# Performance work log

Hardware: AMD Instinct MI355X
Metric: run time of the kernel (lower is better)

The kernel has to match this reference:

```python
import jax, jax.numpy as jnp
import numpy as np

L, N, D, T = 24, 576, 4096, 128
RED = D // 4           # DSU reduced dim (reduction_ratio=4)
FOCUS = (-2) % L       # focus layer index = 22
EPS_LN = 1e-5          # torch LayerNorm default eps
EPS_SC = 1e-6          # score-normalization eps
N_FOCUS = 32           # final_focus (hardcoded in forward)
N_NONFOCUS = 32        # final_nonfocus (hardcoded in forward)
MIN_ACTIVE = 8
THRESH = 3.0


def _ln(x, g=None, b=None):
    mu = x.mean(-1, keepdims=True)
    var = ((x - mu) ** 2).mean(-1, keepdims=True)
    y = (x - mu) / jnp.sqrt(var + EPS_LN)
    if g is not None:
        y = y * g + b
    return y


def setup_inputs() -> dict:
    key = jax.random.key(0)
    ks = jax.random.split(key, 10)
    rn = lambda k, shape, s=0.02: jax.random.normal(k, shape, jnp.float32) * s
    z = lambda n: jnp.zeros((n,), jnp.float32)
    return {
        'text_features': jax.random.normal(ks[0], (T, D), jnp.float32),
        'layer_feats': jax.random.normal(ks[1], (L, N, D), jnp.float32),
        'W1': rn(ks[2], (RED, 3 * D)), 'b1': z(RED),
        'Wc': rn(ks[3], (D, RED)), 'bc_lin': z(D), 'bc': z(D),
        'Wi': rn(ks[4], (D, RED)), 'bi_lin': z(D), 'bi': z(D),
        'Wf': rn(ks[5], (D, RED)), 'bf_lin': z(D), 'bf': z(D),
        'score_q_w': rn(ks[6], (D, D)), 'score_k_w': rn(ks[7], (D, D)),
        'ln_g': jnp.ones((D,), jnp.float32), 'ln_b': z(D),
        'layer_logits': rn(ks[8], (L,), 0.1),
        'scale': jnp.array([0.1], jnp.float32),
    }


def reference(text_features, layer_feats, W1, b1, Wc, bc_lin, bc, Wi, bi_lin, bi,
              Wf, bf_lin, bf, score_q_w, score_k_w, ln_g, ln_b, layer_logits, scale):
    # --- text conditioning ---
    text_global = _ln(text_features.mean(0))                 # [D]
    y = layer_feats.mean(1)                                   # [L, D] per-layer pooled

    # --- DSU recurrence over layers (LSTM-like cell) ---
    def dsu(c_prev, y_l):
        comb = jnp.concatenate([jax.nn.sigmoid(c_prev), y_l, text_global])
        s = jax.nn.relu(W1 @ comb + b1)                       # [RED]
        c_t = jnp.tanh(Wc @ s + bc_lin + bc)
        i = jax.nn.sigmoid(Wi @ s + bi_lin + bi)
        f = jax.nn.sigmoid(Wf @ s + bf_lin + bf)
        c = f * c_prev + i * c_t
        return c, c

    _, ctx = jax.lax.scan(dsu, jnp.zeros((D,), text_features.dtype), y)  # [L, D]

    # --- per-layer scores with LayerNorm'd q/k ---
    q = _ln(ctx @ score_q_w.T, ln_g, ln_b)                    # [L, D]
    kf = _ln(layer_feats @ score_k_w.T, ln_g, ln_b)           # [L, N, D]
    raw = jnp.einsum('lnd,ld->ln', kf, q)                     # [L, N]
    mu = raw.mean(1, keepdims=True)
    sd = raw.std(1, keepdims=True) + EPS_SC                   # unbiased=False
    scores = (raw - mu) / sd                                  # [L, N]
    conf = scores.max(1)                                      # [L]

    # --- active-layer selection (threshold path vs top-8 fallback) ---
    nonfocus = jnp.ones((L,), bool).at[FOCUS].set(False)
    conf_nf = jnp.where(nonfocus, conf, -jnp.inf)
    act_t = nonfocus & (conf > THRESH)
    M_t = act_t.sum()
    _, idx_f = jax.lax.top_k(conf_nf, MIN_ACTIVE)             # fallback: top-8 conf, desc
    act_f = jnp.zeros((L,), bool).at[idx_f].set(True)
    pos_f = jnp.full((L,), L, jnp.int32).at[idx_f].set(jnp.arange(MIN_ACTIVE, dtype=jnp.int32))
    pos_t = jnp.cumsum(act_t.astype(jnp.int32)) - 1           # ascending layer order
    use_fb = M_t < MIN_ACTIVE
    act = jnp.where(use_fb, act_f, act_t)
    pos = jnp.where(use_fb, pos_f, pos_t)
    M = jnp.where(use_fb, MIN_ACTIVE, M_t)

    # --- budget split: base per active layer + remainder to earliest (N=576 >> 32, no deficit) ---
    base = N_NONFOCUS // M
    rem = N_NONFOCUS - base * M
    k_nf = jnp.where(act, base + (pos < rem).astype(jnp.int32), 0)  # [L], sums to 32

    # --- per-layer top-32 indices (sorted desc), gather evidence ---
    _, top_idx = jax.lax.top_k(scores, N_FOCUS)               # [L, 32]
    ev_focus = layer_feats[FOCUS][top_idx[FOCUS]]             # [32, D]
    cum = jnp.cumsum(k_nf)                                    # [L]
    t = jnp.arange(N_NONFOCUS)
    li = jnp.searchsorted(cum, t, side='right')               # owning layer per slot
    r = t - (cum[li] - k_nf[li])                              # rank within layer
    ev_nf = layer_feats[li, top_idx[li, r]]                   # [32, D]

    # --- anchor-residual layer mix + 3x3 group pooling ---
    logits = layer_logits.astype(jnp.float32).at[FOCUS].set(-jnp.inf)
    alpha = jax.nn.softmax(logits)                            # [L], alpha[anchor]=0
    anchor = layer_feats[FOCUS]                               # [N, D]
    delta = jnp.einsum('l,lnd->nd', alpha, layer_feats - anchor[None])
    x_mix = anchor + scale[0] * delta                         # [576, D]
    groups = x_mix.reshape(3, 8, 3, 8, D).transpose(0, 2, 1, 3, 4).reshape(9, 64, D).mean(1)

    return jnp.concatenate([ev_focus, ev_nf, groups], 0)      # [73, D]
```

## Files before the change

kernel.cpp:

```cpp
#include <hip/hip_runtime.h>
#include <stdint.h>
#include <math.h>

#define LAY 24
#define NTOK 576
#define DIM 4096
#define TTXT 128
#define REDD 1024
#define FOCUSL 22

typedef unsigned int u32;
typedef unsigned short u16;
typedef float f32x4 __attribute__((ext_vector_type(4)));
typedef short bf16x8 __attribute__((ext_vector_type(8)));
typedef u16 u16x4 __attribute__((ext_vector_type(4)));

__device__ __forceinline__ u16 f2bf(float f) {
  u32 u = __builtin_bit_cast(u32, f);
  u32 r = u + 0x7fffu + ((u >> 16) & 1u);
  return (u16)(r >> 16);
}
__device__ __forceinline__ float sigm(float x) { return 1.0f / (1.0f + expf(-x)); }

__global__ void k_text_colmean(const float* __restrict__ tf, float* __restrict__ tmean) {
  int c = blockIdx.x * 256 + threadIdx.x;
  float s = 0.f;
  for (int r = 0; r < TTXT; r++) s += tf[(size_t)r * DIM + c];
  tmean[c] = s * (1.0f / TTXT);
}

__global__ void k_text_ln(const float* __restrict__ tmean, float* __restrict__ tg) {
  __shared__ float red[256];
  int t = threadIdx.x;
  float x[16]; float s = 0.f;
  for (int i = 0; i < 16; i++) { x[i] = tmean[i * 256 + t]; s += x[i]; }
  red[t] = s; __syncthreads();
  for (int o = 128; o; o >>= 1) { if (t < o) red[t] += red[t + o]; __syncthreads(); }
  float mean = red[0] / DIM; __syncthreads();
  float q = 0.f;
  for (int i = 0; i < 16; i++) { float d = x[i] - mean; q += d * d; }
  red[t] = q; __syncthreads();
  for (int o = 128; o; o >>= 1) { if (t < o) red[t] += red[t + o]; __syncthreads(); }
  float var = red[0] / DIM;
  float rinv = 1.0f / sqrtf(var + 1e-5f);
  for (int i = 0; i < 16; i++) tg[i * 256 + t] = (x[i] - mean) * rinv;
}

__global__ void k_pass_a(const float* __restrict__ x, u16* __restrict__ xb,
                         float* __restrict__ gm) {
  int bid = blockIdx.x;
  int a = bid % 3, dc = (bid / 3) & 3, l = bid / 12;
  int d4 = dc * 1024 + threadIdx.x * 4;
  f32x4 acc[3] = {};
  int n0 = a * 192;
  const float* p = x + ((size_t)(l * NTOK + n0)) * DIM + d4;
  u16* q = xb + ((size_t)(l * NTOK + n0)) * DIM + d4;
  for (int nn = 0; nn < 192; nn++) {
    f32x4 v = *(const f32x4*)p;
    u16x4 bv; bv.x = f2bf(v.x); bv.y = f2bf(v.y); bv.z = f2bf(v.z); bv.w = f2bf(v.w);
    *(u16x4*)q = bv;
    int c = (nn >> 3) % 3;
    acc[c] += v;
    p += DIM; q += DIM;
  }
  for (int c = 0; c < 3; c++) {
    f32x4 o = acc[c] * (1.0f / 64.0f);
    *(f32x4*)(gm + ((size_t)(l * 9 + a * 3 + c)) * DIM + d4) = o;
  }
}

__global__ void k_y(const float* __restrict__ gm, float* __restrict__ y) {
  int bid = blockIdx.x;
  int l = bid >> 2, dc = bid & 3;
  int d4 = dc * 1024 + threadIdx.x * 4;
  f32x4 s = {};
  for (int g = 0; g < 9; g++) s += *(const f32x4*)(gm + ((size_t)(l * 9 + g)) * DIM + d4);
  *(f32x4*)(y + (size_t)l * DIM + d4) = s * (1.0f / 9.0f);
}

__global__ void k_conv_wk(const float* __restrict__ wk, u16* __restrict__ wkb) {
  size_t i = (size_t)blockIdx.x * 256 + threadIdx.x;
  f32x4 v = ((const f32x4*)wk)[i];
  u16x4 b; b.x = f2bf(v.x); b.y = f2bf(v.y); b.z = f2bf(v.z); b.w = f2bf(v.w);
  ((u16x4*)wkb)[i] = b;
}

__global__ __launch_bounds__(256) void k_gemm_s2(const u16* __restrict__ xb,
                                                 const u16* __restrict__ wkb,
                                                 float* __restrict__ s2p) {
  __shared__ __align__(16) u16 As[128 * 32];
  __shared__ __align__(16) u16 Bs[128 * 32];
  int bid = blockIdx.x;
  int mt = bid >> 5, nt = bid & 31;
  int tid = threadIdx.x;
  int wid = tid >> 6, lane = tid & 63;
  int wm = (wid >> 1) * 64, wn = (wid & 1) * 64;
  int lm = lane & 15, qq = lane >> 4;
  f32x4 acc[4][4] = {};
  const u16* gA = xb + (size_t)(mt * 128) * DIM;
  const u16* gB = wkb + (size_t)(nt * 128) * DIM;
  for (int kt = 0; kt < DIM / 32; kt++) {
    int k0 = kt * 32;
    bf16x8 av[2], bv[2];
    for (int j = 0; j < 2; j++) {
      int seg = tid + 256 * j;
      int row = seg >> 2, ko = (seg & 3) * 8;
      av[j] = *(const bf16x8*)(gA + (size_t)row * DIM + k0 + ko);
      bv[j] = *(const bf16x8*)(gB + (size_t)row * DIM + k0 + ko);
    }
    __syncthreads();
    for (int j = 0; j < 2; j++) {
      int seg = tid + 256 * j;
      *(bf16x8*)&As[seg * 8] = av[j];
      *(bf16x8*)&Bs[seg * 8] = bv[j];
    }
    __syncthreads();
    bf16x8 aF[4], bF[4];
    for (int mi = 0; mi < 4; mi++) aF[mi] = *(const bf16x8*)&As[(wm + mi * 16 + lm) * 32 + qq * 8];
    for (int ni = 0; ni < 4; ni++) bF[ni] = *(const bf16x8*)&Bs[(wn + ni * 16 + lm) * 32 + qq * 8];
    for (int mi = 0; mi < 4; mi++)
      for (int ni = 0; ni < 4; ni++)
        acc[mi][ni] = __builtin_amdgcn_mfma_f32_16x16x32_bf16(aF[mi], bF[ni], acc[mi][ni], 0, 0, 0);
  }
  for (int mi = 0; mi < 4; mi++) {
    for (int reg = 0; reg < 4; reg++) {
      float s = 0.f;
      for (int ni = 0; ni < 4; ni++) { float v = acc[mi][ni][reg]; s += v * v; }
      for (int off = 1; off < 16; off <<= 1) s += __shfl_xor(s, off, 64);
      if (lm == 0) {
        int row = mt * 128 + wm + mi * 16 + qq * 4 + reg;
        s2p[(size_t)row * 64 + nt * 2 + (wid & 1)] = s;
      }
    }
  }
}

__global__ void k_s2_reduce(const float* __restrict__ s2p, float* __restrict__ S2) {
  int row = blockIdx.x * 256 + threadIdx.x;
  const f32x4* p = (const f32x4*)(s2p + (size_t)row * 64);
  float s = 0.f;
  for (int i = 0; i < 16; i++) { f32x4 v = p[i]; s += v.x + v.y + v.z + v.w; }
  S2[row] = s;
}

__global__ __launch_bounds__(256) void k_pre(const float* __restrict__ W1, const float* __restrict__ b1,
                                             const float* __restrict__ y, const float* __restrict__ tg,
                                             float* __restrict__ pre) {
  int r = blockIdx.x, t = threadIdx.x;
  __shared__ float ylds[LAY][256];
  __shared__ float tglds[256];
  __shared__ float red[256];
  float acc[LAY]; for (int l = 0; l < LAY; l++) acc[l] = 0.f;
  float accc = 0.f;
  const float* wb = W1 + (size_t)r * (3 * DIM) + DIM;
  const float* wc = W1 + (size_t)r * (3 * DIM) + 2 * DIM;
  for (int ch = 0; ch < 16; ch++) {
    for (int l = 0; l < LAY; l++) ylds[l][t] = y[(size_t)l * DIM + ch * 256 + t];
    tglds[t] = tg[ch * 256 + t];
    __syncthreads();
    float w1b = wb[ch * 256 + t];
    float w1c = wc[ch * 256 + t];
    for (int l = 0; l < LAY; l++) acc[l] += w1b * ylds[l][t];
    accc += w1c * tglds[t];
    __syncthreads();
  }
  red[t] = accc; __syncthreads();
  for (int o = 128; o; o >>= 1) { if (t < o) red[t] += red[t + o]; __syncthreads(); }
  float csum = red[0]; __syncthreads();
  for (int l = 0; l < LAY; l++) {
    red[t] = acc[l]; __syncthreads();
    for (int o = 128; o; o >>= 1) { if (t < o) red[t] += red[t + o]; __syncthreads(); }
    if (t == 0) pre[l * REDD + r] = b1[r] + red[0] + csum;
    __syncthreads();
  }
}

__global__ void k_dsu_init(float* __restrict__ c_prev, float* __restrict__ u) {
  int i = blockIdx.x * 256 + threadIdx.x;
  c_prev[i] = 0.0f;
  u[i] = 0.5f;
}

__global__ __launch_bounds__(256) void k_dsu1(const float* __restrict__ W1, const float* __restrict__ pre,
                                              const float* __restrict__ u, float* __restrict__ svec,
                                              int l) {
  __shared__ __align__(16) float ulds[DIM];
  int b = blockIdx.x, t = threadIdx.x;
  int wid = t >> 6, lane = t & 63;
  for (int i = 0; i < 16; i++) ulds[i * 256 + t] = u[i * 256 + t];
  __syncthreads();
  int r = b * 4 + wid;
  const float* wrow = W1 + (size_t)r * (3 * DIM);
  float acc = 0.f;
  for (int i = 0; i < 16; i++) {
    int e = i * 256 + lane * 4;
    f32x4 w = *(const f32x4*)(wrow + e);
    f32x4 uv = *(const f32x4*)(&ulds[e]);
    acc += w.x * uv.x + w.y * uv.y + w.z * uv.z + w.w * uv.w;
  }
  for (int off = 32; off; off >>= 1) acc += __shfl_down(acc, off, 64);
  if (lane == 0) {
    float sv = acc + pre[l * REDD + r];
    svec[r] = sv > 0.f ? sv : 0.f;
  }
}

__global__ __launch_bounds__(256) void k_dsu2(
    const float* __restrict__ Wc, const float* __restrict__ Wi, const float* __restrict__ Wf,
    const float* __restrict__ bc_lin, const float* __restrict__ bc,
    const float* __restrict__ bi_lin, const float* __restrict__ bi,
    const float* __restrict__ bf_lin, const float* __restrict__ bf,
    const float* __restrict__ svec, float* __restrict__ c_prev, float* __restrict__ u,
    float* __restrict__ ctx, int l) {
  __shared__ __align__(16) float sl[REDD];
  int b = blockIdx.x, t = threadIdx.x;
  int wid = t >> 6, lane = t & 63;
  for (int i = 0; i < 4; i++) sl[i * 256 + t] = svec[i * 256 + t];
  __syncthreads();
  int d = b * 4 + wid;
  float g3[3];
  for (int gate = 0; gate < 3; gate++) {
    const float* wrow = (gate == 0 ? Wc : (gate == 1 ? Wi : Wf)) + (size_t)d * REDD;
    float acc = 0.f;
    for (int i = 0; i < 4; i++) {
      int k = i * 256 + lane * 4;
      f32x4 w = *(const f32x4*)(wrow + k);
      f32x4 sv = *(const f32x4*)(&sl[k]);
      acc += w.x * sv.x + w.y * sv.y + w.z * sv.z + w.w * sv.w;
    }
    for (int off = 32; off; off >>= 1) acc += __shfl_down(acc, off, 64);
    g3[gate] = acc;
  }
  if (lane == 0) {
    float ct = tanhf(g3[0] + bc_lin[d] + bc[d]);
    float iv = sigm(g3[1] + bi_lin[d] + bi[d]);
    float fv = sigm(g3[2] + bf_lin[d] + bf[d]);
    float c = fv * c_prev[d] + iv * ct;
    c_prev[d] = c;
    u[d] = sigm(c);
    ctx[(size_t)l * DIM + d] = c;
  }
}

__global__ __launch_bounds__(256) void k_qpre(const float* __restrict__ ctx, const float* __restrict__ Wq,
                                              float* __restrict__ qpre) {
  __shared__ __align__(16) float clds[LAY][512];
  int b = blockIdx.x, t = threadIdx.x;
  int wid = t >> 6, lane = t & 63;
  int e = b * 4 + wid;
  const float* wrow = Wq + (size_t)e * DIM;
  float acc[LAY]; for (int l = 0; l < LAY; l++) acc[l] = 0.f;
  for (int ch = 0; ch < 8; ch++) {
    for (int i = 0; i < 48; i++) {
      int idx = i * 256 + t;
      int l = idx >> 9, dd = idx & 511;
      clds[l][dd] = ctx[(size_t)l * DIM + ch * 512 + dd];
    }
    __syncthreads();
    for (int i = 0; i < 2; i++) {
      int dd = i * 256 + lane * 4;
      f32x4 w = *(const f32x4*)(wrow + ch * 512 + dd);
      for (int l = 0; l < LAY; l++) {
        f32x4 c = *(const f32x4*)(&clds[l][dd]);
        acc[l] += w.x * c.x + w.y * c.y + w.z * c.z + w.w * c.w;
      }
    }
    __syncthreads();
  }
  for (int l = 0; l < LAY; l++) {
    float s = acc[l];
    for (int off = 32; off; off >>= 1) s += __shfl_down(s, off, 64);
    if (lane == 0) qpre[(size_t)l * DIM + e] = s;
  }
}

__global__ void k_qln(const float* __restrict__ qpre, const float* __restrict__ g, const float* __restrict__ bb,
                      float* __restrict__ h, float* __restrict__ A, float* __restrict__ Bv) {
  int l = blockIdx.x, t = threadIdx.x;
  __shared__ float red[256];
  float x[16]; float s = 0.f;
  for (int i = 0; i < 16; i++) { x[i] = qpre[(size_t)l * DIM + i * 256 + t]; s += x[i]; }
  red[t] = s; __syncthreads();
  for (int o = 128; o; o >>= 1) { if (t < o) red[t] += red[t + o]; __syncthreads(); }
  float mean = red[0] / DIM; __syncthreads();
  float qs = 0.f;
  for (int i = 0; i < 16; i++) { float dd = x[i] - mean; qs += dd * dd; }
  red[t] = qs; __syncthreads();
  for (int o = 128; o; o >>= 1) { if (t < o) red[t] += red[t + o]; __syncthreads(); }
  float var = red[0] / DIM;
  float rinv = 1.0f / sqrtf(var + 1e-5f);
  float sa = 0.f, sb = 0.f;
  for (int i = 0; i < 16; i++) {
    int d = i * 256 + t;
    float gv = g[d], bv = bb[d];
    float qv = (x[i] - mean) * rinv * gv + bv;
    float hv = gv * qv;
    h[(size_t)l * DIM + d] = hv;
    sa += hv; sb += bv * qv;
  }
  __syncthreads();
  red[t] = sa; __syncthreads();
  for (int o = 128; o; o >>= 1) { if (t < o) red[t] += red[t + o]; __syncthreads(); }
  if (t == 0) A[l] = red[0];
  __syncthreads();
  red[t] = sb; __syncthreads();
  for (int o = 128; o; o >>= 1) { if (t < o) red[t] += red[t + o]; __syncthreads(); }
  if (t == 0) Bv[l] = red[0];
}

__global__ __launch_bounds__(256) void k_v(const float* __restrict__ Wk, const float* __restrict__ h,
                                           float* __restrict__ v, float* __restrict__ wmu) {
  int eb = blockIdx.x & 15, db = blockIdx.x >> 4;
  int t = threadIdx.x;
  __shared__ float hl[LAY][256];
  for (int l = 0; l < LAY; l++) hl[l][t] = h[(size_t)l * DIM + db * 256 + t];
  __syncthreads();
  int e = eb * 256 + t;
  float acc[LAY]; for (int l = 0; l < LAY; l++) acc[l] = 0.f;
  float am = 0.f;
  for (int dd = 0; dd < 256; dd++) {
    float w = Wk[(size_t)(db * 256 + dd) * DIM + e];
    am += w;
    for (int l = 0; l < LAY; l++) acc[l] += w * hl[l][dd];
  }
  for (int l = 0; l < LAY; l++) atomicAdd(&v[(size_t)l * DIM + e], acc[l]);
  atomicAdd(&wmu[e], am * (1.0f / DIM));
}

__global__ __launch_bounds__(256) void k_dotmu(const float* __restrict__ x, const float* __restrict__ v,
                                               const float* __restrict__ wmu, float* __restrict__ dotv,
                                               float* __restrict__ muv) {
  __shared__ __align__(16) float vl[DIM];
  __shared__ __align__(16) float wm[DIM];
  int bid = blockIdx.x;
  int l = bid / 144, n4 = bid % 144;
  int t = threadIdx.x, wid = t >> 6, lane = t & 63;
  for (int i = 0; i < 16; i++) {
    int idx = i * 256 + t;
    vl[idx] = v[(size_t)l * DIM + idx];
    wm[idx] = wmu[idx];
  }
  __syncthreads();
  int n = n4 * 4 + wid;
  const float* row = x + (size_t)(l * NTOK + n) * DIM;
  float ad = 0.f, am = 0.f;
  for (int i = 0; i < 16; i++) {
    int e = i * 256 + lane * 4;
    f32x4 xv = *(const f32x4*)(row + e);
    f32x4 vv = *(const f32x4*)(&vl[e]);
    f32x4 wv = *(const f32x4*)(&wm[e]);
    ad += xv.x * vv.x + xv.y * vv.y + xv.z * vv.z + xv.w * vv.w;
    am += xv.x * wv.x + xv.y * wv.y + xv.z * wv.z + xv.w * wv.w;
  }
  for (int off = 32; off; off >>= 1) { ad += __shfl_down(ad, off, 64); am += __shfl_down(am, off, 64); }
  if (lane == 0) { dotv[l * NTOK + n] = ad; muv[l * NTOK + n] = am; }
}

__global__ void k_scores(const float* __restrict__ dotv, const float* __restrict__ muv,
                         const float* __restrict__ S2, const float* __restrict__ A, const float* __restrict__ Bv,
                         int* __restrict__ topidx, float* __restrict__ conf) {
  int l = blockIdx.x, t = threadIdx.x;
  __shared__ float raw[NTOK];
  __shared__ float rv[256]; __shared__ int ri[256];
  float Al = A[l], Bl = Bv[l];
  for (int j = t; j < NTOK; j += 256) {
    float dv = dotv[l * NTOK + j], mv = muv[l * NTOK + j];
    float var = S2[l * NTOK + j] * (1.0f / DIM) - mv * mv;
    float sd = sqrtf(var + 1e-5f);
    raw[j] = (dv - mv * Al) / sd + Bl;
  }
  __syncthreads();
  float s = 0.f;
  for (int j = t; j < NTOK; j += 256) s += raw[j];
  rv[t] = s; __syncthreads();
  for (int o = 128; o; o >>= 1) { if (t < o) rv[t] += rv[t + o]; __syncthreads(); }
  float mean = rv[0] / NTOK; __syncthreads();
  float qsum = 0.f;
  for (int j = t; j < NTOK; j += 256) { float d = raw[j] - mean; qsum += d * d; }
  rv[t] = qsum; __syncthreads();
  for (int o = 128; o; o >>= 1) { if (t < o) rv[t] += rv[t + o]; __syncthreads(); }
  float sdn = sqrtf(rv[0] / NTOK) + 1e-6f; __syncthreads();
  for (int k = 0; k < 32; k++) {
    float bvv = -INFINITY; int bii = NTOK;
    for (int j = t; j < NTOK; j += 256) {
      float vv = raw[j];
      if (vv > bvv || (vv == bvv && j < bii)) { bvv = vv; bii = j; }
    }
    rv[t] = bvv; ri[t] = bii; __syncthreads();
    for (int o = 128; o; o >>= 1) {
      if (t < o) {
        if (rv[t + o] > rv[t] || (rv[t + o] == rv[t] && ri[t + o] < ri[t])) { rv[t] = rv[t + o]; ri[t] = ri[t + o]; }
      }
      __syncthreads();
    }
    if (t == 0) {
      topidx[l * 32 + k] = ri[0];
      if (k == 0) conf[l] = (rv[0] - mean) / sdn;
      raw[ri[0]] = -INFINITY;
    }
    __syncthreads();
  }
}

__global__ void k_select(const float* __restrict__ conf, const int* __restrict__ topidx,
                         const float* __restrict__ logits,
                         int* __restrict__ src, float* __restrict__ alpha) {
  if (threadIdx.x != 0 || blockIdx.x != 0) return;
  float cf[LAY]; for (int l = 0; l < LAY; l++) cf[l] = conf[l];
  bool actt[LAY]; int Mt = 0;
  for (int l = 0; l < LAY; l++) { actt[l] = (l != FOCUSL) && (cf[l] > 3.0f); if (actt[l]) Mt++; }
  bool act[LAY]; int pos[LAY]; int M;
  if (Mt < 8) {
    float cnf[LAY];
    for (int l = 0; l < LAY; l++) cnf[l] = (l == FOCUSL) ? -INFINITY : cf[l];
    bool used[LAY] = {};
    for (int l = 0; l < LAY; l++) { act[l] = false; pos[l] = LAY; }
    for (int j = 0; j < 8; j++) {
      float bv = -INFINITY; int bidx = -1;
      for (int l = 0; l < LAY; l++) if (!used[l] && cnf[l] > bv) { bv = cnf[l]; bidx = l; }
      used[bidx] = true; act[bidx] = true; pos[bidx] = j;
    }
    M = 8;
  } else {
    int c = 0;
    for (int l = 0; l < LAY; l++) { act[l] = actt[l]; if (actt[l]) { pos[l] = c; c++; } else pos[l] = -1; }
    M = Mt;
  }
  int base = 32 / M, rem = 32 - base * M;
  int kk[LAY]; int cum[LAY]; int run = 0;
  for (int l = 0; l < LAY; l++) {
    int k = act[l] ? (base + ((pos[l] < rem) ? 1 : 0)) : 0;
    kk[l] = k; run += k; cum[l] = run;
  }
  for (int tt = 0; tt < 32; tt++) src[tt] = FOCUSL * NTOK + topidx[FOCUSL * 32 + tt];
  for (int tt = 0; tt < 32; tt++) {
    int li = 0;
    while (cum[li] <= tt) li++;
    int r = tt - (cum[li] - kk[li]);
    src[32 + tt] = li * NTOK + topidx[li * 32 + r];
  }
  float mx = -INFINITY;
  for (int l = 0; l < LAY; l++) if (l != FOCUSL && logits[l] > mx) mx = logits[l];
  float ssum = 0.f; float av[LAY];
  for (int l = 0; l < LAY; l++) { av[l] = (l == FOCUSL) ? 0.0f : expf(logits[l] - mx); ssum += av[l]; }
  for (int l = 0; l < LAY; l++) alpha[l] = av[l] / ssum;
}

__global__ void k_gather(const float* __restrict__ x, const int* __restrict__ src, float* __restrict__ out) {
  int b = blockIdx.x, t = threadIdx.x;
  const float* row = x + (size_t)src[b] * DIM;
  float* o = out + (size_t)b * DIM;
  for (int i = 0; i < 4; i++) {
    int e = (i * 256 + t) * 4;
    *(f32x4*)(o + e) = *(const f32x4*)(row + e);
  }
}

__global__ void k_groups(const float* __restrict__ gm, const float* __restrict__ alpha,
                         const float* __restrict__ scale, float* __restrict__ out) {
  int g = blockIdx.x, t = threadIdx.x;
  float sc = scale[0];
  __shared__ float al[LAY];
  if (t < LAY) al[t] = alpha[t];
  __syncthreads();
  for (int i = 0; i < 4; i++) {
    int d = (i * 256 + t) * 4;
    f32x4 mix = {};
    for (int l = 0; l < LAY; l++) {
      f32x4 gv = *(const f32x4*)(gm + ((size_t)(l * 9 + g)) * DIM + d);
      mix += gv * al[l];
    }
    f32x4 anc = *(const f32x4*)(gm + ((size_t)(FOCUSL * 9 + g)) * DIM + d);
    f32x4 o = anc + (mix - anc) * sc;
    *(f32x4*)(out + (size_t)(64 + g) * DIM + d) = o;
  }
}

extern "C" void kernel_launch(void* const* d_in, const int* in_sizes, int n_in,
                              void* d_out, int out_size, void* d_ws, size_t ws_size,
                              hipStream_t stream) {
  const float* tf     = (const float*)d_in[0];
  const float* x      = (const float*)d_in[1];
  const float* W1     = (const float*)d_in[2];
  const float* b1     = (const float*)d_in[3];
  const float* Wc     = (const float*)d_in[4];
  const float* bc_lin = (const float*)d_in[5];
  const float* bc     = (const float*)d_in[6];
  const float* Wi     = (const float*)d_in[7];
  const float* bi_lin = (const float*)d_in[8];
  const float* bi     = (const float*)d_in[9];
  const float* Wf     = (const float*)d_in[10];
  const float* bf_lin = (const float*)d_in[11];
  const float* bf     = (const float*)d_in[12];
  const float* Wq     = (const float*)d_in[13];
  const float* Wk     = (const float*)d_in[14];
  const float* ln_g   = (const float*)d_in[15];
  const float* ln_b   = (const float*)d_in[16];
  const float* logits = (const float*)d_in[17];
  const float* scale  = (const float*)d_in[18];
  float* out = (float*)d_out;

  char* w = (char*)d_ws;
  size_t off = 0;
  auto alloc = [&](size_t bytes) -> void* {
    void* p = w + off;
    off += (bytes + 255) & ~(size_t)255;
    return p;
  };
  float* v    = (float*)alloc((size_t)LAY * DIM * 4);
  float* wmu  = (float*)alloc((size_t)DIM * 4);
  size_t zero_bytes = off;
  u16* xb     = (u16*)alloc((size_t)LAY * NTOK * DIM * 2);
  u16* wkb    = (u16*)alloc((size_t)DIM * DIM * 2);
  float* gm   = (float*)alloc((size_t)LAY * 9 * DIM * 4);
  float* y    = (float*)alloc((size_t)LAY * DIM * 4);
  float* tmean= (float*)alloc((size_t)DIM * 4);
  float* tg   = (float*)alloc((size_t)DIM * 4);
  float* pre  = (float*)alloc((size_t)LAY * REDD * 4);
  float* svec = (float*)alloc((size_t)REDD * 4);
  float* cprev= (float*)alloc((size_t)DIM * 4);
  float* uvec = (float*)alloc((size_t)DIM * 4);
  float* ctx  = (float*)alloc((size_t)LAY * DIM * 4);
  float* qpre = (float*)alloc((size_t)LAY * DIM * 4);
  float* h    = (float*)alloc((size_t)LAY * DIM * 4);
  float* A    = (float*)alloc((size_t)LAY * 4);
  float* Bv   = (float*)alloc((size_t)LAY * 4);
  float* s2p  = (float*)alloc((size_t)LAY * NTOK * 64 * 4);
  float* S2   = (float*)alloc((size_t)LAY * NTOK * 4);
  float* dotv = (float*)alloc((size_t)LAY * NTOK * 4);
  float* muv  = (float*)alloc((size_t)LAY * NTOK * 4);
  int* topidx = (int*)alloc((size_t)LAY * 32 * 4);
  float* conf = (float*)alloc((size_t)LAY * 4);
  int* src    = (int*)alloc(64 * 4);
  float* alph = (float*)alloc((size_t)LAY * 4);
  (void)in_sizes; (void)n_in; (void)out_size; (void)ws_size;

  hipMemsetAsync(d_ws, 0, zero_bytes, stream);
  k_text_colmean<<<16, 256, 0, stream>>>(tf, tmean);
  k_text_ln<<<1, 256, 0, stream>>>(tmean, tg);
  k_pass_a<<<288, 256, 0, stream>>>(x, xb, gm);
  k_y<<<96, 256, 0, stream>>>(gm, y);
  k_conv_wk<<<16384, 256, 0, stream>>>(Wk, wkb);
  k_gemm_s2<<<108 * 32, 256, 0, stream>>>(xb, wkb, s2p);
  k_s2_reduce<<<54, 256, 0, stream>>>(s2p, S2);
  k_pre<<<1024, 256, 0, stream>>>(W1, b1, y, tg, pre);
  k_dsu_init<<<16, 256, 0, stream>>>(cprev, uvec);
  for (int l = 0; l < LAY; l++) {
    k_dsu1<<<256, 256, 0, stream>>>(W1, pre, uvec, svec, l);
    k_dsu2<<<1024, 256, 0, stream>>>(Wc, Wi, Wf, bc_lin, bc, bi_lin, bi, bf_lin, bf,
                                     svec, cprev, uvec, ctx, l);
  }
  k_qpre<<<1024, 256, 0, stream>>>(ctx, Wq, qpre);
  k_qln<<<24, 256, 0, stream>>>(qpre, ln_g, ln_b, h, A, Bv);
  k_v<<<256, 256, 0, stream>>>(Wk, h, v, wmu);
  k_dotmu<<<24 * 144, 256, 0, stream>>>(x, v, wmu, dotv, muv);
  k_scores<<<24, 256, 0, stream>>>(dotv, muv, S2, A, Bv, topidx, conf);
  k_select<<<1, 64, 0, stream>>>(conf, topidx, logits, src, alph);
  k_gather<<<64, 256, 0, stream>>>(x, src, out);
  k_groups<<<9, 256, 0, stream>>>(gm, alph, scale, out);
}
```

Measured before the change: 2.119 ms.

## Use direct global-to-LDS loads in GEMM, regrid pass_a, warp-shuffle top-k

```diff
diff --git a/kernel.cpp b/kernel.cpp
--- a/kernel.cpp
+++ b/kernel.cpp
@@ -22,6 +22,12 @@
 }
 __device__ __forceinline__ float sigm(float x) { return 1.0f / (1.0f + expf(-x)); }
 
+#define GLOBAL_AS __attribute__((address_space(1)))
+#define LDS_AS __attribute__((address_space(3)))
+__device__ __forceinline__ void gld_lds16(const void* g, void* l) {
+  __builtin_amdgcn_global_load_lds((const GLOBAL_AS u32*)g, (LDS_AS u32*)l, 16, 0, 0);
+}
+
 __global__ void k_text_colmean(const float* __restrict__ tf, float* __restrict__ tmean) {
   int c = blockIdx.x * 256 + threadIdx.x;
   float s = 0.f;
@@ -49,8 +55,8 @@
 __global__ void k_pass_a(const float* __restrict__ x, u16* __restrict__ xb,
                          float* __restrict__ gm) {
   int bid = blockIdx.x;
-  int a = bid % 3, dc = (bid / 3) & 3, l = bid / 12;
-  int d4 = dc * 1024 + threadIdx.x * 4;
+  int a = bid % 3, dc = (bid / 3) & 7, l = bid / 24;
+  int d4 = dc * 512 + threadIdx.x * 4;
   f32x4 acc[3] = {};
   int n0 = a * 192;
   const float* p = x + ((size_t)(l * NTOK + n0)) * DIM + d4;
@@ -101,18 +107,12 @@
   const u16* gB = wkb + (size_t)(nt * 128) * DIM;
   for (int kt = 0; kt < DIM / 32; kt++) {
     int k0 = kt * 32;
-    bf16x8 av[2], bv[2];
+    __syncthreads();
     for (int j = 0; j < 2; j++) {
       int seg = tid + 256 * j;
       int row = seg >> 2, ko = (seg & 3) * 8;
-      av[j] = *(const bf16x8*)(gA + (size_t)row * DIM + k0 + ko);
-      bv[j] = *(const bf16x8*)(gB + (size_t)row * DIM + k0 + ko);
-    }
-    __syncthreads();
-    for (int j = 0; j < 2; j++) {
-      int seg = tid + 256 * j;
-      *(bf16x8*)&As[seg * 8] = av[j];
-      *(bf16x8*)&Bs[seg * 8] = bv[j];
+      gld_lds16(gA + (size_t)row * DIM + k0 + ko, &As[seg * 8]);
+      gld_lds16(gB + (size_t)row * DIM + k0 + ko, &Bs[seg * 8]);
     }
     __syncthreads();
     bf16x8 aF[4], bF[4];
@@ -361,7 +361,9 @@
                          int* __restrict__ topidx, float* __restrict__ conf) {
   int l = blockIdx.x, t = threadIdx.x;
   __shared__ float raw[NTOK];
-  __shared__ float rv[256]; __shared__ int ri[256];
+  __shared__ float rv[256];
+  __shared__ float wv4[4]; __shared__ int wi4[4];
+  int wid = t >> 6, lane = t & 63;
   float Al = A[l], Bl = Bv[l];
   for (int j = t; j < NTOK; j += 256) {
     float dv = dotv[l * NTOK + j], mv = muv[l * NTOK + j];
@@ -381,22 +383,24 @@
   for (int o = 128; o; o >>= 1) { if (t < o) rv[t] += rv[t + o]; __syncthreads(); }
   float sdn = sqrtf(rv[0] / NTOK) + 1e-6f; __syncthreads();
   for (int k = 0; k < 32; k++) {
-    float bvv = -INFINITY; int bii = NTOK;
+    float bv = -INFINITY; int bi = NTOK;
     for (int j = t; j < NTOK; j += 256) {
       float vv = raw[j];
-      if (vv > bvv || (vv == bvv && j < bii)) { bvv = vv; bii = j; }
-    }
-    rv[t] = bvv; ri[t] = bii; __syncthreads();
-    for (int o = 128; o; o >>= 1) {
-      if (t < o) {
-        if (rv[t + o] > rv[t] || (rv[t + o] == rv[t] && ri[t + o] < ri[t])) { rv[t] = rv[t + o]; ri[t] = ri[t + o]; }
-      }
-      __syncthreads();
-    }
+      if (vv > bv || (vv == bv && j < bi)) { bv = vv; bi = j; }
+    }
+    for (int off = 32; off; off >>= 1) {
+      float ov = __shfl_down(bv, off, 64); int oi = __shfl_down(bi, off, 64);
+      if (ov > bv || (ov == bv && oi < bi)) { bv = ov; bi = oi; }
+    }
+    if (lane == 0) { wv4[wid] = bv; wi4[wid] = bi; }
+    __syncthreads();
     if (t == 0) {
-      topidx[l * 32 + k] = ri[0];
-      if (k == 0) conf[l] = (rv[0] - mean) / sdn;
-      raw[ri[0]] = -INFINITY;
+      float b2 = wv4[0]; int i2 = wi4[0];
+      for (int w2 = 1; w2 < 4; w2++)
+        if (wv4[w2] > b2 || (wv4[w2] == b2 && wi4[w2] < i2)) { b2 = wv4[w2]; i2 = wi4[w2]; }
+      topidx[l * 32 + k] = i2;
+      if (k == 0) conf[l] = (b2 - mean) / sdn;
+      raw[i2] = -INFINITY;
     }
     __syncthreads();
   }
@@ -538,7 +542,7 @@
   hipMemsetAsync(d_ws, 0, zero_bytes, stream);
   k_text_colmean<<<16, 256, 0, stream>>>(tf, tmean);
   k_text_ln<<<1, 256, 0, stream>>>(tmean, tg);
-  k_pass_a<<<288, 256, 0, stream>>>(x, xb, gm);
+  k_pass_a<<<576, 128, 0, stream>>>(x, xb, gm);
   k_y<<<96, 256, 0, stream>>>(gm, y);
   k_conv_wk<<<16384, 256, 0, stream>>>(Wk, wkb);
   k_gemm_s2<<<108 * 32, 256, 0, stream>>>(xb, wkb, s2p);
```

After: 2.055 ms. 3.0% less time.
